# Kernel tuning notes

Hardware: AMD Instinct MI355X
Metric: run time of the kernel (lower is better)

The kernel has to match this reference:

```python
import jax, jax.numpy as jnp
import numpy as np

B = 16
C = 80
LEVELS = [(128, 128, 8), (64, 64, 16), (32, 32, 32), (16, 16, 64), (8, 8, 128)]
TOPN = 1000
MIN_SCORE = 0.05
NMS_THR = 0.6
MAX_OBJ = 100


def setup_inputs() -> dict:
    key = jax.random.key(0)
    inp = {}
    for l, (H, W, s) in enumerate(LEVELS):
        key, k1, k2, k3 = jax.random.split(key, 4)
        inp[f"cls{l}"] = jax.random.uniform(k1, (B, H, W, C), jnp.float32)
        inp[f"reg{l}"] = jax.random.uniform(k2, (B, H, W, 4), jnp.float32) * 128.0
        inp[f"ctr{l}"] = jax.random.uniform(k3, (B, H, W, 1), jnp.float32)
        xs = (jnp.arange(W, dtype=jnp.float32) + 0.5) * s
        ys = (jnp.arange(H, dtype=jnp.float32) + 0.5) * s
        gx, gy = jnp.meshgrid(xs, ys)  # [H, W]
        pos = jnp.stack([gx, gy], axis=-1)  # [H, W, 2]
        inp[f"pos{l}"] = jnp.broadcast_to(pos, (B, H, W, 2))
    return inp


def _nms_one(scores, classes, bboxes):
    # scores [N], classes int32 [N], bboxes float [N, 4] (already int-truncated values)
    s = jnp.where(scores > MIN_SCORE, scores, -jnp.inf)  # score-threshold mask
    top_s, top_i = jax.lax.top_k(s, TOPN)  # sort descending, keep topn
    top_c = jax.lax.stop_gradient(classes[top_i].astype(jnp.float32))
    top_b = bboxes[top_i]
    valid = top_s > MIN_SCORE
    wh = top_b[:, 2:4] - top_b[:, 0:2]
    areas = jnp.clip(wh[:, 0] * wh[:, 1], 0.0001)
    ar = jnp.arange(TOPN)

    def body(i, suppressed):
        active = valid[i] & (~suppressed[i])
        b = top_b[i]
        tl = jnp.maximum(b[0:2], top_b[:, 0:2])
        br = jnp.minimum(b[2:4], top_b[:, 2:4])
        owh = jnp.clip(br - tl, 0.0)
        inter = owh[:, 0] * owh[:, 1]
        union = jnp.clip(areas[i] + areas - inter, 0.0001)
        iou = inter / union
        return suppressed | (active & (ar > i) & (iou >= NMS_THR))

    suppressed = jax.lax.fori_loop(0, TOPN, body, jnp.zeros((TOPN,), bool))
    keep = valid & (~suppressed)
    rank = jnp.cumsum(keep.astype(jnp.int32)) - 1
    # scatter kept detections (in score order) into first MAX_OBJ slots; slot MAX_OBJ is a dump
    idx = jnp.where(keep & (rank < MAX_OBJ), rank, MAX_OBJ)
    out_s = jnp.full((MAX_OBJ + 1,), -1.0, jnp.float32).at[idx].set(jnp.where(keep, top_s, -1.0))[:MAX_OBJ]
    out_c = jnp.full((MAX_OBJ + 1,), -1.0, jnp.float32).at[idx].set(jnp.where(keep, top_c, -1.0))[:MAX_OBJ]
    out_b = jnp.zeros((MAX_OBJ + 1, 4), jnp.float32).at[idx].set(jnp.where(keep[:, None], top_b, 0.0))[:MAX_OBJ]
    return out_s, out_c, out_b


def _forward(cls_list, reg_list, ctr_list, pos_list):
    ss, cc, bb = [], [], []
    for c, r, t, p in zip(cls_list, reg_list, ctr_list, pos_list):
        b = c.shape[0]
        c = c.reshape(b, -1, c.shape[-1])   # [B, HW, 80]
        r = r.reshape(b, -1, 4)             # [B, HW, 4]
        t = t.reshape(b, -1)                # [B, HW]
        p = p.reshape(b, -1, 2)             # [B, HW, 2]
        sc = jnp.sqrt(jnp.max(c, axis=2) * t)
        cl = jnp.argmax(c, axis=2).astype(jnp.int32)
        bmin = p - r[:, :, 0:2]
        bmax = p + r[:, :, 2:4]
        # torch .int() truncates toward zero; values are used as floats afterward
        box = jax.lax.stop_gradient(jnp.trunc(jnp.concatenate([bmin, bmax], axis=2)))
        ss.append(sc); cc.append(cl); bb.append(box)
    scores = jnp.concatenate(ss, axis=1)
    classes = jnp.concatenate(cc, axis=1)
    boxes = jnp.concatenate(bb, axis=1)
    return jax.vmap(_nms_one)(scores, classes, boxes)


def reference(cls0, cls1, cls2, cls3, cls4, reg0, reg1, reg2, reg3, reg4,
              ctr0, ctr1, ctr2, ctr3, ctr4, pos0, pos1, pos2, pos3, pos4):
    return _forward([cls0, cls1, cls2, cls3, cls4],
                    [reg0, reg1, reg2, reg3, reg4],
                    [ctr0, ctr1, ctr2, ctr3, ctr4],
                    [pos0, pos1, pos2, pos3, pos4])
```

## Files before the change

kernel.cpp:

```cpp
#include <hip/hip_runtime.h>
#include <stdint.h>

typedef unsigned int u32;
typedef unsigned long long u64;

#define NTOT 21824
#define NBATCH 16
#define TOPN 1000
#define MAXOBJ 100
#define CAP 2048
#define CAPC 8192

__global__ void zero_kernel(u32* __restrict__ h) {
    int i = blockIdx.x * 1024 + threadIdx.x;
    if (i < NBATCH * 2048 + NBATCH * 32) h[i] = 0;
}

__global__ __launch_bounds__(256) void decode_kernel(
    const float* __restrict__ cls0, const float* __restrict__ cls1,
    const float* __restrict__ cls2, const float* __restrict__ cls3,
    const float* __restrict__ cls4,
    const float* __restrict__ ctr0, const float* __restrict__ ctr1,
    const float* __restrict__ ctr2, const float* __restrict__ ctr3,
    const float* __restrict__ ctr4,
    u32* __restrict__ keys, int* __restrict__ clsidx,
    u32* __restrict__ hist0)
{
    __shared__ u32 bh[2048];
    for (int i = threadIdx.x; i < 2048; i += 256) bh[i] = 0;
    __syncthreads();

    int tid = threadIdx.x;
    int g = tid >> 2, j = tid & 3;
    int loc = blockIdx.x * 64 + g;
    int b = blockIdx.y;
    if (loc < NTOT) {
        const float *cp, *tp;
        if (loc < 16384)      { size_t o = (size_t)b*16384 + loc;          cp = cls0 + o*80; tp = ctr0 + o; }
        else if (loc < 20480) { size_t o = (size_t)b*4096  + (loc-16384);  cp = cls1 + o*80; tp = ctr1 + o; }
        else if (loc < 21504) { size_t o = (size_t)b*1024  + (loc-20480);  cp = cls2 + o*80; tp = ctr2 + o; }
        else if (loc < 21760) { size_t o = (size_t)b*256   + (loc-21504);  cp = cls3 + o*80; tp = ctr3 + o; }
        else                  { size_t o = (size_t)b*64    + (loc-21760);  cp = cls4 + o*80; tp = ctr4 + o; }

        const float4* c4 = (const float4*)cp;
        float maxv = -1.0f; int arg = 0;
#pragma unroll
        for (int q = 0; q < 5; ++q) {
            float4 v = c4[j + 4*q];
            int ch = 16*q + 4*j;
            if (v.x > maxv) { maxv = v.x; arg = ch;     }
            if (v.y > maxv) { maxv = v.y; arg = ch + 1; }
            if (v.z > maxv) { maxv = v.z; arg = ch + 2; }
            if (v.w > maxv) { maxv = v.w; arg = ch + 3; }
        }
#pragma unroll
        for (int d = 1; d <= 2; d <<= 1) {
            float ov = __shfl_xor(maxv, d);
            int   oa = __shfl_xor(arg, d);
            if (ov > maxv || (ov == maxv && oa < arg)) { maxv = ov; arg = oa; }
        }
        if (j == 0) {
            float score = sqrtf(maxv * (*tp));
            u32 key = (score > 0.05f) ? (__float_as_uint(score) | 0x80000000u) : 0u;
            size_t o = (size_t)b * NTOT + loc;
            keys[o] = key;
            clsidx[o] = arg;
            if (key) atomicAdd(&bh[key >> 21], 1u);
        }
    }
    __syncthreads();
    for (int i = threadIdx.x; i < 2048; i += 256) {
        u32 c = bh[i];
        if (c) atomicAdd(&hist0[b * 2048 + i], c);
    }
}

__global__ __launch_bounds__(1024) void pivot_kernel(
    const u32* __restrict__ keys, const u32* __restrict__ hist0,
    u32* __restrict__ params,
    float* __restrict__ tscore, float* __restrict__ tcls, float4* __restrict__ tbox)
{
    __shared__ u32 shist[2048];
    __shared__ u32 s_wtot[16];
    __shared__ int s_tf;
    __shared__ u32 s_C, s_above;
    int b = blockIdx.x, tid = threadIdx.x;
    int lane = tid & 63, wave = tid >> 6;
    const u32* kb = keys + (size_t)b * NTOT;

    for (int i = tid; i < TOPN; i += 1024) {
        size_t o = (size_t)b * TOPN + i;
        tscore[o] = -1.0f; tcls[o] = -1.0f;
        tbox[o] = make_float4(0.f, 0.f, 0.f, 0.f);
    }

    u32 h0 = hist0[b * 2048 + 2 * tid];
    u32 h1 = hist0[b * 2048 + 2 * tid + 1];
    if (tid == 0) s_tf = -1;
    u32 x = h0 + h1;
#pragma unroll
    for (int off = 1; off < 64; off <<= 1) {
        u32 y = __shfl_down(x, off);
        if (lane + off < 64) x += y;
    }
    if (lane == 0) s_wtot[wave] = x;
    __syncthreads();
    u32 wsuf = 0, tot = 0;
    for (int w2 = 0; w2 < 16; ++w2) { u32 v = s_wtot[w2]; tot += v; if (w2 > wave) wsuf += v; }
    u32 suf0 = x + wsuf, suf1 = suf0 - h0;
    u32 target = (tot < TOPN) ? tot : TOPN;

    if (target > 0) {
        if (suf0 >= target) atomicMax(&s_tf, 2 * tid);
        if (suf1 >= target) atomicMax(&s_tf, 2 * tid + 1);
    }
    __syncthreads();
    int t0 = s_tf;
    if (target > 0) {
        if (2 * tid == t0)     { s_C = suf0; s_above = suf0 - h0; }
        if (2 * tid + 1 == t0) { s_C = suf1; s_above = suf1 - h1; }
    }
    __syncthreads();
    u32 C0 = (target > 0) ? s_C : 0;
    u32 above0 = (target > 0) ? s_above : 0;

    bool need2 = (target > 0 && C0 > CAP);
    int t1 = 0; u32 C1 = 0, above1 = 0;
    shist[2 * tid] = 0; shist[2 * tid + 1] = 0;
    if (tid == 0) s_tf = -1;
    __syncthreads();
    if (need2) {
        for (int i = tid; i < NTOT; i += 1024) {
            u32 k = kb[i];
            if (k && (int)(k >> 21) == t0) atomicAdd(&shist[(k >> 10) & 2047], 1u);
        }
    }
    __syncthreads();
    {
        u32 g0 = shist[2 * tid], g1 = shist[2 * tid + 1];
        u32 x2 = g0 + g1;
#pragma unroll
        for (int off = 1; off < 64; off <<= 1) {
            u32 y = __shfl_down(x2, off);
            if (lane + off < 64) x2 += y;
        }
        if (lane == 0) s_wtot[wave] = x2;
        __syncthreads();
        u32 ws2 = 0;
        for (int w2 = wave + 1; w2 < 16; ++w2) ws2 += s_wtot[w2];
        u32 sa0 = x2 + ws2, sa1 = sa0 - g0;
        u32 need2c = target - above0;
        if (need2) {
            if (sa0 >= need2c) atomicMax(&s_tf, 2 * tid);
            if (sa1 >= need2c) atomicMax(&s_tf, 2 * tid + 1);
        }
        __syncthreads();
        t1 = s_tf;
        if (need2) {
            if (2 * tid == t1)     { s_C = above0 + sa0; s_above = above0 + sa0 - g0; }
            if (2 * tid + 1 == t1) { s_C = above0 + sa1; s_above = above0 + sa1 - g1; }
        }
        __syncthreads();
        if (need2) { C1 = s_C; above1 = s_above; }
    }

    bool need3 = (need2 && C1 > CAP);
    int t2 = 0;
    __syncthreads();
    shist[2 * tid] = 0; shist[2 * tid + 1] = 0;
    if (tid == 0) s_tf = -1;
    __syncthreads();
    if (need3) {
        for (int i = tid; i < NTOT; i += 1024) {
            u32 k = kb[i];
            if (k && (int)(k >> 21) == t0 && (int)((k >> 10) & 2047) == t1)
                atomicAdd(&shist[k & 1023], 1u);
        }
    }
    __syncthreads();
    {
        u32 g = shist[tid];
        u32 x3 = g;
#pragma unroll
        for (int off = 1; off < 64; off <<= 1) {
            u32 y = __shfl_down(x3, off);
            if (lane + off < 64) x3 += y;
        }
        if (lane == 0) s_wtot[wave] = x3;
        __syncthreads();
        u32 ws3 = 0;
        for (int w2 = wave + 1; w2 < 16; ++w2) ws3 += s_wtot[w2];
        u32 sb = x3 + ws3;
        if (need3) {
            u32 need3c = target - above1;
            if (sb >= need3c && tid < 1024) atomicMax(&s_tf, tid);
        }
        __syncthreads();
        t2 = s_tf;
    }

    if (tid == 0) {
        u32 P;
        if (target == 0)      P = 0xFFFFFFFFu;
        else if (!need2)      P = (u32)t0 << 21;
        else if (!need3)      P = ((u32)t0 << 21) | ((u32)t1 << 10);
        else                  P = ((u32)t0 << 21) | ((u32)t1 << 10) | (u32)t2;
        params[2 * b] = P;
        params[2 * b + 1] = target;
    }
}

__global__ __launch_bounds__(256) void gather_kernel(
    const u32* __restrict__ keys, const u32* __restrict__ params,
    u64* __restrict__ candbuf, u32* __restrict__ gcnt)
{
    __shared__ u32 s_wcnt[4];
    __shared__ u32 s_base;
    int b = blockIdx.y;
    int tid = threadIdx.x;
    int lane = tid & 63, wave = tid >> 6;
    u32 P = params[2 * b];
    int i = blockIdx.x * 256 + tid;
    u32 k = (i < NTOT) ? keys[(size_t)b * NTOT + i] : 0u;
    bool pass = (k != 0u) && (k >= P);
    u64 mask = __ballot(pass);
    if (lane == 0) s_wcnt[wave] = (u32)__popcll(mask);
    __syncthreads();
    if (tid == 0) {
        u32 tot = s_wcnt[0] + s_wcnt[1] + s_wcnt[2] + s_wcnt[3];
        s_base = tot ? atomicAdd(&gcnt[b * 32], tot) : 0u;
    }
    __syncthreads();
    if (pass) {
        u32 woff = 0;
        for (int w2 = 0; w2 < wave; ++w2) woff += s_wcnt[w2];
        u32 pos = s_base + woff + (u32)__popcll(mask & ((1ull << lane) - 1ull));
        if (pos < CAPC)
            candbuf[(size_t)b * CAPC + pos] = ((u64)k << 32) | (u32)(~i);
    }
}

__global__ __launch_bounds__(256) void rank_kernel(
    const u64* __restrict__ candbuf, const u32* __restrict__ gcnt,
    const u32* __restrict__ params,
    const int* __restrict__ clsidx,
    const float* __restrict__ reg0, const float* __restrict__ reg1,
    const float* __restrict__ reg2, const float* __restrict__ reg3,
    const float* __restrict__ reg4,
    float* __restrict__ tscore, float* __restrict__ tcls, float4* __restrict__ tbox)
{
    int b = blockIdx.y;
    int lane = threadIdx.x & 63;
    u32 M = gcnt[b * 32]; if (M > CAPC) M = CAPC;
    u32 target = params[2 * b + 1];
    const u64* cb = candbuf + (size_t)b * CAPC;
    u32 Mr = (M + 63u) & ~63u;

    u32 wbase0 = blockIdx.x * 256 + (threadIdx.x & ~63u);
    for (u32 base = wbase0; base < M; base += 8 * 256) {
        u32 i0 = base + lane;
        bool val = (i0 < M);
        u64 e = val ? cb[i0] : ~0ull;
        u32 r = 0;
        for (u32 c0 = 0; c0 < Mr; c0 += 64) {
            u32 j = c0 + lane;
            u64 v = (j < M) ? cb[j] : 0ull;
            u32 vlo = (u32)v, vhi = (u32)(v >> 32);
#pragma unroll
            for (int s = 0; s < 64; ++s) {
                u32 lo = (u32)__builtin_amdgcn_readlane((int)vlo, s);
                u32 hi = (u32)__builtin_amdgcn_readlane((int)vhi, s);
                u64 vj = ((u64)hi << 32) | lo;
                r += (vj > e) ? 1u : 0u;
            }
        }
        if (val && r < target) {
            u32 k = (u32)(e >> 32);
            u32 loc = ~(u32)e;
            const float* rp; float st; u32 li; int wsh;
            if (loc < 16384u)      { li = loc;          wsh = 7; st = 8.f;   rp = reg0 + ((size_t)b*16384 + li)*4; }
            else if (loc < 20480u) { li = loc - 16384u; wsh = 6; st = 16.f;  rp = reg1 + ((size_t)b*4096  + li)*4; }
            else if (loc < 21504u) { li = loc - 20480u; wsh = 5; st = 32.f;  rp = reg2 + ((size_t)b*1024  + li)*4; }
            else if (loc < 21760u) { li = loc - 21504u; wsh = 4; st = 64.f;  rp = reg3 + ((size_t)b*256   + li)*4; }
            else                   { li = loc - 21760u; wsh = 3; st = 128.f; rp = reg4 + ((size_t)b*64    + li)*4; }
            u32 wx = li & ((1u << wsh) - 1u);
            u32 hy = li >> wsh;
            float px = ((float)wx + 0.5f) * st;
            float py = ((float)hy + 0.5f) * st;
            float4 rg = *(const float4*)rp;
            float4 bx;
            bx.x = truncf(px - rg.x); bx.y = truncf(py - rg.y);
            bx.z = truncf(px + rg.z); bx.w = truncf(py + rg.w);
            size_t src = (size_t)b * NTOT + loc;
            size_t o = (size_t)b * TOPN + r;
            tscore[o] = __uint_as_float(k & 0x7FFFFFFFu);
            tcls[o] = (float)clsidx[src];
            tbox[o] = bx;
        }
    }
}

__global__ __launch_bounds__(256) void iou_kernel(
    const float4* __restrict__ tbox, u64* __restrict__ sup)
{
    __shared__ float4 sbox[TOPN];
    int b = blockIdx.y;
    int tid = threadIdx.x, lane = tid & 63, wave = tid >> 6;
    const float4* tb = tbox + (size_t)b * TOPN;
    for (int i = tid; i < TOPN; i += 256) sbox[i] = tb[i];
    __syncthreads();
    int i = blockIdx.x * 4 + wave;
    float4 bi = sbox[i];
    float areai = fmaxf((bi.z - bi.x) * (bi.w - bi.y), 0.0001f);
    u64* row = sup + ((size_t)b * TOPN + i) * 16;
#pragma unroll
    for (int w = 0; w < 16; ++w) {
        int col = w * 64 + lane;
        bool bit = false;
        if (col < TOPN) {
            float4 bj = sbox[col];
            float areaj = fmaxf((bj.z - bj.x) * (bj.w - bj.y), 0.0001f);
            float tlx = fmaxf(bi.x, bj.x), tly = fmaxf(bi.y, bj.y);
            float brx = fminf(bi.z, bj.z), bry = fminf(bi.w, bj.w);
            float ow = fmaxf(brx - tlx, 0.f), oh = fmaxf(bry - tly, 0.f);
            float inter = ow * oh;
            float uni = fmaxf(areai + areaj - inter, 0.0001f);
            bit = (col > i) && (inter / uni >= 0.6f);
        }
        u64 m = __ballot(bit);
        if (lane == 0) row[w] = m;
    }
}

#define CHROWS 128
#define NCHUNK 8

__global__ __launch_bounds__(1024) void finalize_kernel(
    const float* __restrict__ tscore, const float* __restrict__ tcls,
    const float4* __restrict__ tbox, const u64* __restrict__ sup,
    float* __restrict__ out)
{
    __shared__ u64 mat[2][CHROWS * 16];
    __shared__ u32 validsh[TOPN];
    __shared__ u64 removed_sh[16];
    __shared__ u32 wpref[17];
    int b = blockIdx.x, tid = threadIdx.x;
    int wave = tid >> 6, lane = tid & 63;

    for (int i = tid; i < TOPN; i += 1024)
        validsh[i] = (tscore[(size_t)b * TOPN + i] > 0.05f) ? 1u : 0u;

    const u64* supb = sup + (size_t)b * TOPN * 16;
    for (int idx = tid; idx < CHROWS * 16; idx += 1024)
        mat[0][idx] = supb[idx];
    __syncthreads();

    u64 my = 0;
    if (wave == 0) {
#pragma unroll
        for (int w2 = 0; w2 < 16; ++w2) {
            int i = w2 * 64 + lane;
            bool v = (i < TOPN) ? (validsh[i] != 0) : false;
            u64 m = __ballot(v);
            if (lane == w2) my = ~m;
        }
    }

    for (int chunk = 0; chunk < NCHUNK; ++chunk) {
        if (wave > 0 && chunk + 1 < NCHUNK) {
            int nr = (chunk + 1 == NCHUNK - 1) ? (TOPN - (NCHUNK - 1) * CHROWS) : CHROWS;
            const u64* src = supb + (size_t)(chunk + 1) * CHROWS * 16;
            u64* dst = mat[(chunk + 1) & 1];
            for (int idx = tid - 64; idx < nr * 16; idx += 960)
                dst[idx] = src[idx];
        }
        if (wave == 0) {
            int r0 = chunk * CHROWS;
            int rows = (chunk == NCHUNK - 1) ? (TOPN - r0) : CHROWS;
            int lw = lane & 15;
            const u64* M = mat[chunk & 1];
            for (int sub = 0; sub < rows; sub += 64) {
                int w2 = (r0 + sub) >> 6;
                u64 cur = __shfl(my, w2);
                int nsub = rows - sub; if (nsub > 64) nsub = 64;
                const u64* R = M + sub * 16;
                int ngrp = nsub >> 3;
                u64 cme[8], cww[8];
#pragma unroll
                for (int g = 0; g < 8; ++g) { cme[g] = R[g*16 + lw]; cww[g] = R[g*16 + w2]; }
                for (int grp = 0; grp < ngrp; ++grp) {
                    u64 nme[8] = {0,0,0,0,0,0,0,0}, nww[8] = {0,0,0,0,0,0,0,0};
                    if (grp + 1 < ngrp) {
                        const u64* Rn = R + (grp + 1) * 128;
#pragma unroll
                        for (int g = 0; g < 8; ++g) { nme[g] = Rn[g*16 + lw]; nww[g] = Rn[g*16 + w2]; }
                    }
#pragma unroll
                    for (int g = 0; g < 8; ++g) {
                        int u = grp * 8 + g;
                        u64 bit = (cur >> u) & 1ull;
                        u64 act = bit - 1ull;
                        cur |= cww[g] & act;
                        my  |= cme[g] & act;
                    }
#pragma unroll
                    for (int g = 0; g < 8; ++g) { cme[g] = nme[g]; cww[g] = nww[g]; }
                }
            }
        }
        __syncthreads();
    }
    if (wave == 0) {
        if (lane < 16) removed_sh[lane] = my;
        u32 pc = (lane < 16) ? (u32)__popcll(~my) : 0u;
#pragma unroll
        for (int off = 1; off < 16; off <<= 1) {
            u32 y = __shfl_up(pc, off);
            if (lane >= off) pc += y;
        }
        if (lane < 16) wpref[lane + 1] = pc;
        if (lane == 0) wpref[0] = 0;
    }
    __syncthreads();

    float* out_s = out;
    float* out_c = out + NBATCH * MAXOBJ;
    float* out_b = out + 2 * NBATCH * MAXOBJ;
    if (tid < MAXOBJ)     { out_s[b * MAXOBJ + tid] = -1.f; out_c[b * MAXOBJ + tid] = -1.f; }
    if (tid < MAXOBJ * 4) out_b[b * MAXOBJ * 4 + tid] = 0.f;
    __syncthreads();
    if (tid < TOPN) {
        u64 kw = ~removed_sh[tid >> 6];
        if ((kw >> (tid & 63)) & 1ull) {
            int rank = (int)wpref[tid >> 6] + (int)__popcll(kw & ((1ull << (tid & 63)) - 1ull));
            if (rank < MAXOBJ) {
                size_t o = (size_t)b * TOPN + tid;
                out_s[b * MAXOBJ + rank] = tscore[o];
                out_c[b * MAXOBJ + rank] = tcls[o];
                ((float4*)out_b)[b * MAXOBJ + rank] = tbox[o];
            }
        }
    }
}

extern "C" void kernel_launch(void* const* d_in, const int* in_sizes, int n_in,
                              void* d_out, int out_size, void* d_ws, size_t ws_size,
                              hipStream_t stream) {
    (void)in_sizes; (void)n_in; (void)out_size; (void)ws_size;
    const float* cls[5]; const float* reg[5]; const float* ctr[5];
    for (int l = 0; l < 5; ++l) {
        cls[l] = (const float*)d_in[4 * l + 0];
        reg[l] = (const float*)d_in[4 * l + 1];
        ctr[l] = (const float*)d_in[4 * l + 2];
    }
    char* w = (char*)d_ws;
    u32*    keys   = (u32*)(w + 0);
    int*    clsidx = (int*)(w + 1396736);
    float*  tscore = (float*)(w + 8380416);
    float*  tcls   = (float*)(w + 8444416);
    float4* tbox   = (float4*)(w + 8508416);
    u64*    sup    = (u64*)(w + 8764416);
    u64*    candbuf= (u64*)(w + 8764416);
    u32*    hist0  = (u32*)(w + 9812992);
    u32*    gcnt   = (u32*)(w + 9944064);
    u32*    params = (u32*)(w + 9946112);

    zero_kernel<<<33, 1024, 0, stream>>>(hist0);
    decode_kernel<<<dim3((NTOT + 63) / 64, NBATCH), 256, 0, stream>>>(
        cls[0], cls[1], cls[2], cls[3], cls[4],
        ctr[0], ctr[1], ctr[2], ctr[3], ctr[4],
        keys, clsidx, hist0);
    pivot_kernel<<<NBATCH, 1024, 0, stream>>>(keys, hist0, params, tscore, tcls, tbox);
    gather_kernel<<<dim3((NTOT + 255) / 256, NBATCH), 256, 0, stream>>>(keys, params, candbuf, gcnt);
    rank_kernel<<<dim3(8, NBATCH), 256, 0, stream>>>(candbuf, gcnt, params, clsidx,
                                                     reg[0], reg[1], reg[2], reg[3], reg[4],
                                                     tscore, tcls, tbox);
    iou_kernel<<<dim3(TOPN / 4, NBATCH), 256, 0, stream>>>(tbox, sup);
    finalize_kernel<<<NBATCH, 1024, 0, stream>>>(tscore, tcls, tbox, sup, (float*)d_out);
}
```

Baseline: 278.0 us.

## Fuse histogram, zeroing and gather into pivot kernel with candidate compaction

Removes the zero kernel and the global histogram atomics from decode. The pivot kernel now builds the first-level histogram itself, using four per-wave-group shared histograms to reduce atomic contention. It then compacts top-bucket candidates into a buffer that later radix passes rescan instead of the full key array, and does the final gather itself. This drops two kernel launches and the global atomics, but puts more serial work onto only 16 blocks.

```diff
diff --git a/kernel.cpp b/kernel.cpp
--- a/kernel.cpp
+++ b/kernel.cpp
@@ -10,11 +10,6 @@
 #define MAXOBJ 100
 #define CAP 2048
 #define CAPC 8192
-
-__global__ void zero_kernel(u32* __restrict__ h) {
-    int i = blockIdx.x * 1024 + threadIdx.x;
-    if (i < NBATCH * 2048 + NBATCH * 32) h[i] = 0;
-}
 
 __global__ __launch_bounds__(256) void decode_kernel(
     const float* __restrict__ cls0, const float* __restrict__ cls1,
@@ -23,70 +18,61 @@
     const float* __restrict__ ctr0, const float* __restrict__ ctr1,
     const float* __restrict__ ctr2, const float* __restrict__ ctr3,
     const float* __restrict__ ctr4,
-    u32* __restrict__ keys, int* __restrict__ clsidx,
-    u32* __restrict__ hist0)
+    u32* __restrict__ keys, int* __restrict__ clsidx)
 {
-    __shared__ u32 bh[2048];
-    for (int i = threadIdx.x; i < 2048; i += 256) bh[i] = 0;
-    __syncthreads();
-
     int tid = threadIdx.x;
     int g = tid >> 2, j = tid & 3;
     int loc = blockIdx.x * 64 + g;
     int b = blockIdx.y;
-    if (loc < NTOT) {
-        const float *cp, *tp;
-        if (loc < 16384)      { size_t o = (size_t)b*16384 + loc;          cp = cls0 + o*80; tp = ctr0 + o; }
-        else if (loc < 20480) { size_t o = (size_t)b*4096  + (loc-16384);  cp = cls1 + o*80; tp = ctr1 + o; }
-        else if (loc < 21504) { size_t o = (size_t)b*1024  + (loc-20480);  cp = cls2 + o*80; tp = ctr2 + o; }
-        else if (loc < 21760) { size_t o = (size_t)b*256   + (loc-21504);  cp = cls3 + o*80; tp = ctr3 + o; }
-        else                  { size_t o = (size_t)b*64    + (loc-21760);  cp = cls4 + o*80; tp = ctr4 + o; }
-
-        const float4* c4 = (const float4*)cp;
-        float maxv = -1.0f; int arg = 0;
-#pragma unroll
-        for (int q = 0; q < 5; ++q) {
-            float4 v = c4[j + 4*q];
-            int ch = 16*q + 4*j;
-            if (v.x > maxv) { maxv = v.x; arg = ch;     }
-            if (v.y > maxv) { maxv = v.y; arg = ch + 1; }
-            if (v.z > maxv) { maxv = v.z; arg = ch + 2; }
-            if (v.w > maxv) { maxv = v.w; arg = ch + 3; }
-        }
-#pragma unroll
-        for (int d = 1; d <= 2; d <<= 1) {
-            float ov = __shfl_xor(maxv, d);
-            int   oa = __shfl_xor(arg, d);
-            if (ov > maxv || (ov == maxv && oa < arg)) { maxv = ov; arg = oa; }
-        }
-        if (j == 0) {
-            float score = sqrtf(maxv * (*tp));
-            u32 key = (score > 0.05f) ? (__float_as_uint(score) | 0x80000000u) : 0u;
-            size_t o = (size_t)b * NTOT + loc;
-            keys[o] = key;
-            clsidx[o] = arg;
-            if (key) atomicAdd(&bh[key >> 21], 1u);
-        }
-    }
-    __syncthreads();
-    for (int i = threadIdx.x; i < 2048; i += 256) {
-        u32 c = bh[i];
-        if (c) atomicAdd(&hist0[b * 2048 + i], c);
+    if (loc >= NTOT) return;
+    const float *cp, *tp;
+    if (loc < 16384)      { size_t o = (size_t)b*16384 + loc;          cp = cls0 + o*80; tp = ctr0 + o; }
+    else if (loc < 20480) { size_t o = (size_t)b*4096  + (loc-16384);  cp = cls1 + o*80; tp = ctr1 + o; }
+    else if (loc < 21504) { size_t o = (size_t)b*1024  + (loc-20480);  cp = cls2 + o*80; tp = ctr2 + o; }
+    else if (loc < 21760) { size_t o = (size_t)b*256   + (loc-21504);  cp = cls3 + o*80; tp = ctr3 + o; }
+    else                  { size_t o = (size_t)b*64    + (loc-21760);  cp = cls4 + o*80; tp = ctr4 + o; }
+
+    const float4* c4 = (const float4*)cp;
+    float maxv = -1.0f; int arg = 0;
+#pragma unroll
+    for (int q = 0; q < 5; ++q) {
+        float4 v = c4[j + 4*q];
+        int ch = 16*q + 4*j;
+        if (v.x > maxv) { maxv = v.x; arg = ch;     }
+        if (v.y > maxv) { maxv = v.y; arg = ch + 1; }
+        if (v.z > maxv) { maxv = v.z; arg = ch + 2; }
+        if (v.w > maxv) { maxv = v.w; arg = ch + 3; }
+    }
+#pragma unroll
+    for (int d = 1; d <= 2; d <<= 1) {
+        float ov = __shfl_xor(maxv, d);
+        int   oa = __shfl_xor(arg, d);
+        if (ov > maxv || (ov == maxv && oa < arg)) { maxv = ov; arg = oa; }
+    }
+    if (j == 0) {
+        float score = sqrtf(maxv * (*tp));
+        u32 key = (score > 0.05f) ? (__float_as_uint(score) | 0x80000000u) : 0u;
+        size_t o = (size_t)b * NTOT + loc;
+        keys[o] = key;
+        clsidx[o] = arg;
     }
 }
 
 __global__ __launch_bounds__(1024) void pivot_kernel(
-    const u32* __restrict__ keys, const u32* __restrict__ hist0,
-    u32* __restrict__ params,
+    const u32* __restrict__ keys,
+    u64* __restrict__ cb, u64* __restrict__ cand2,
+    u32* __restrict__ gcnt, u32* __restrict__ params,
     float* __restrict__ tscore, float* __restrict__ tcls, float4* __restrict__ tbox)
 {
-    __shared__ u32 shist[2048];
+    __shared__ u32 h4[4][2048];
     __shared__ u32 s_wtot[16];
     __shared__ int s_tf;
-    __shared__ u32 s_C, s_above;
+    __shared__ u32 s_C, s_above, s_cnt;
     int b = blockIdx.x, tid = threadIdx.x;
-    int lane = tid & 63, wave = tid >> 6;
+    int lane = tid & 63, wave = tid >> 6, sub = wave & 3;
     const u32* kb = keys + (size_t)b * NTOT;
+    u64* cbb = cb + (size_t)b * CAPC;
+    u64* c2b = cand2 + (size_t)b * CAPC;
 
     for (int i = tid; i < TOPN; i += 1024) {
         size_t o = (size_t)b * TOPN + i;
@@ -94,9 +80,16 @@
         tbox[o] = make_float4(0.f, 0.f, 0.f, 0.f);
     }
 
-    u32 h0 = hist0[b * 2048 + 2 * tid];
-    u32 h1 = hist0[b * 2048 + 2 * tid + 1];
-    if (tid == 0) s_tf = -1;
+    for (int i = tid; i < 4 * 2048; i += 1024) ((u32*)h4)[i] = 0;
+    if (tid == 0) { s_tf = -1; s_cnt = 0; }
+    __syncthreads();
+    for (int i = tid; i < NTOT; i += 1024) {
+        u32 k = kb[i];
+        if (k) atomicAdd(&h4[sub][k >> 21], 1u);
+    }
+    __syncthreads();
+    u32 h0 = h4[0][2*tid] + h4[1][2*tid] + h4[2][2*tid] + h4[3][2*tid];
+    u32 h1 = h4[0][2*tid+1] + h4[1][2*tid+1] + h4[2][2*tid+1] + h4[3][2*tid+1];
     u32 x = h0 + h1;
 #pragma unroll
     for (int off = 1; off < 64; off <<= 1) {
@@ -109,7 +102,6 @@
     for (int w2 = 0; w2 < 16; ++w2) { u32 v = s_wtot[w2]; tot += v; if (w2 > wave) wsuf += v; }
     u32 suf0 = x + wsuf, suf1 = suf0 - h0;
     u32 target = (tot < TOPN) ? tot : TOPN;
-
     if (target > 0) {
         if (suf0 >= target) atomicMax(&s_tf, 2 * tid);
         if (suf1 >= target) atomicMax(&s_tf, 2 * tid + 1);
@@ -123,21 +115,49 @@
     __syncthreads();
     u32 C0 = (target > 0) ? s_C : 0;
     u32 above0 = (target > 0) ? s_above : 0;
+    bool useCand = (C0 <= CAPC);
+
+    for (int base = 0; base < NTOT; base += 1024) {
+        int i = base + tid;
+        u32 k = (i < NTOT) ? kb[i] : 0u;
+        bool pass = (target > 0) && k && ((int)(k >> 21) >= t0);
+        u64 mask = __ballot(pass);
+        u32 wcnt = (u32)__popcll(mask);
+        u32 wbase = 0;
+        if (lane == 0 && wcnt) wbase = atomicAdd(&s_cnt, wcnt);
+        wbase = __shfl(wbase, 0);
+        if (pass) {
+            u32 pos = wbase + (u32)__popcll(mask & ((1ull << lane) - 1ull));
+            if (pos < CAPC) cbb[pos] = ((u64)k << 32) | (u32)(~i);
+        }
+    }
+    __syncthreads();
+    u32 C0g = s_cnt; (void)C0g;
+    __syncthreads();
+    if (tid == 0) s_cnt = 0;
 
     bool need2 = (target > 0 && C0 > CAP);
     int t1 = 0; u32 C1 = 0, above1 = 0;
-    shist[2 * tid] = 0; shist[2 * tid + 1] = 0;
+    for (int i = tid; i < 4 * 2048; i += 1024) ((u32*)h4)[i] = 0;
     if (tid == 0) s_tf = -1;
     __syncthreads();
     if (need2) {
-        for (int i = tid; i < NTOT; i += 1024) {
-            u32 k = kb[i];
-            if (k && (int)(k >> 21) == t0) atomicAdd(&shist[(k >> 10) & 2047], 1u);
+        if (useCand) {
+            for (u32 i = tid; i < C0; i += 1024) {
+                u32 k = (u32)(cbb[i] >> 32);
+                if ((int)(k >> 21) == t0) atomicAdd(&h4[sub][(k >> 10) & 2047], 1u);
+            }
+        } else {
+            for (int i = tid; i < NTOT; i += 1024) {
+                u32 k = kb[i];
+                if (k && (int)(k >> 21) == t0) atomicAdd(&h4[sub][(k >> 10) & 2047], 1u);
+            }
         }
     }
     __syncthreads();
     {
-        u32 g0 = shist[2 * tid], g1 = shist[2 * tid + 1];
+        u32 g0 = h4[0][2*tid] + h4[1][2*tid] + h4[2][2*tid] + h4[3][2*tid];
+        u32 g1 = h4[0][2*tid+1] + h4[1][2*tid+1] + h4[2][2*tid+1] + h4[3][2*tid+1];
         u32 x2 = g0 + g1;
 #pragma unroll
         for (int off = 1; off < 64; off <<= 1) {
@@ -167,20 +187,29 @@
     bool need3 = (need2 && C1 > CAP);
     int t2 = 0;
     __syncthreads();
-    shist[2 * tid] = 0; shist[2 * tid + 1] = 0;
+    for (int i = tid; i < 4 * 2048; i += 1024) ((u32*)h4)[i] = 0;
     if (tid == 0) s_tf = -1;
     __syncthreads();
     if (need3) {
-        for (int i = tid; i < NTOT; i += 1024) {
-            u32 k = kb[i];
-            if (k && (int)(k >> 21) == t0 && (int)((k >> 10) & 2047) == t1)
-                atomicAdd(&shist[k & 1023], 1u);
+        if (useCand) {
+            for (u32 i = tid; i < C0; i += 1024) {
+                u32 k = (u32)(cbb[i] >> 32);
+                if ((int)(k >> 21) == t0 && (int)((k >> 10) & 2047) == t1)
+                    atomicAdd(&h4[sub][k & 1023], 1u);
+            }
+        } else {
+            for (int i = tid; i < NTOT; i += 1024) {
+                u32 k = kb[i];
+                if (k && (int)(k >> 21) == t0 && (int)((k >> 10) & 2047) == t1)
+                    atomicAdd(&h4[sub][k & 1023], 1u);
+            }
         }
     }
     __syncthreads();
     {
-        u32 g = shist[tid];
-        u32 x3 = g;
+        u32 g0 = h4[0][2*tid] + h4[1][2*tid] + h4[2][2*tid] + h4[3][2*tid];
+        u32 g1 = h4[0][2*tid+1] + h4[1][2*tid+1] + h4[2][2*tid+1] + h4[3][2*tid+1];
+        u32 x3 = g0 + g1;
 #pragma unroll
         for (int off = 1; off < 64; off <<= 1) {
             u32 y = __shfl_down(x3, off);
@@ -190,58 +219,65 @@
         __syncthreads();
         u32 ws3 = 0;
         for (int w2 = wave + 1; w2 < 16; ++w2) ws3 += s_wtot[w2];
-        u32 sb = x3 + ws3;
+        u32 sb0 = x3 + ws3, sb1 = sb0 - g0;
         if (need3) {
             u32 need3c = target - above1;
-            if (sb >= need3c && tid < 1024) atomicMax(&s_tf, tid);
+            if (sb0 >= need3c) atomicMax(&s_tf, 2 * tid);
+            if (sb1 >= need3c) atomicMax(&s_tf, 2 * tid + 1);
         }
         __syncthreads();
         t2 = s_tf;
     }
 
+    u32 P;
+    if (target == 0) P = 0xFFFFFFFFu;
+    else if (!need2) P = (u32)t0 << 21;
+    else if (!need3) P = ((u32)t0 << 21) | ((u32)t1 << 10);
+    else             P = ((u32)t0 << 21) | ((u32)t1 << 10) | (u32)t2;
+
+    if (useCand) {
+        u32 Cr = (C0 + 1023u) & ~1023u;
+        for (u32 base = 0; base < Cr; base += 1024) {
+            u32 i = base + tid;
+            u64 e = 0; bool pass = false;
+            if (i < C0 && target > 0) { e = cbb[i]; pass = ((u32)(e >> 32) >= P); }
+            u64 mask = __ballot(pass);
+            u32 wcnt = (u32)__popcll(mask);
+            u32 wbase = 0;
+            if (lane == 0 && wcnt) wbase = atomicAdd(&s_cnt, wcnt);
+            wbase = __shfl(wbase, 0);
+            if (pass) {
+                u32 pos = wbase + (u32)__popcll(mask & ((1ull << lane) - 1ull));
+                if (pos < CAPC) c2b[pos] = e;
+            }
+        }
+    } else {
+        for (int base = 0; base < NTOT; base += 1024) {
+            int i = base + tid;
+            u32 k = (i < NTOT) ? kb[i] : 0u;
+            bool pass = (target > 0) && k && (k >= P);
+            u64 mask = __ballot(pass);
+            u32 wcnt = (u32)__popcll(mask);
+            u32 wbase = 0;
+            if (lane == 0 && wcnt) wbase = atomicAdd(&s_cnt, wcnt);
+            wbase = __shfl(wbase, 0);
+            if (pass) {
+                u32 pos = wbase + (u32)__popcll(mask & ((1ull << lane) - 1ull));
+                if (pos < CAPC) c2b[pos] = ((u64)k << 32) | (u32)(~i);
+            }
+        }
+    }
+    __syncthreads();
     if (tid == 0) {
-        u32 P;
-        if (target == 0)      P = 0xFFFFFFFFu;
-        else if (!need2)      P = (u32)t0 << 21;
-        else if (!need3)      P = ((u32)t0 << 21) | ((u32)t1 << 10);
-        else                  P = ((u32)t0 << 21) | ((u32)t1 << 10) | (u32)t2;
+        u32 M = s_cnt; if (M > CAPC) M = CAPC;
+        gcnt[b * 32] = M;
         params[2 * b] = P;
         params[2 * b + 1] = target;
     }
 }
 
-__global__ __launch_bounds__(256) void gather_kernel(
-    const u32* __restrict__ keys, const u32* __restrict__ params,
-    u64* __restrict__ candbuf, u32* __restrict__ gcnt)
-{
-    __shared__ u32 s_wcnt[4];
-    __shared__ u32 s_base;
-    int b = blockIdx.y;
-    int tid = threadIdx.x;
-    int lane = tid & 63, wave = tid >> 6;
-    u32 P = params[2 * b];
-    int i = blockIdx.x * 256 + tid;
-    u32 k = (i < NTOT) ? keys[(size_t)b * NTOT + i] : 0u;
-    bool pass = (k != 0u) && (k >= P);
-    u64 mask = __ballot(pass);
-    if (lane == 0) s_wcnt[wave] = (u32)__popcll(mask);
-    __syncthreads();
-    if (tid == 0) {
-        u32 tot = s_wcnt[0] + s_wcnt[1] + s_wcnt[2] + s_wcnt[3];
-        s_base = tot ? atomicAdd(&gcnt[b * 32], tot) : 0u;
-    }
-    __syncthreads();
-    if (pass) {
-        u32 woff = 0;
-        for (int w2 = 0; w2 < wave; ++w2) woff += s_wcnt[w2];
-        u32 pos = s_base + woff + (u32)__popcll(mask & ((1ull << lane) - 1ull));
-        if (pos < CAPC)
-            candbuf[(size_t)b * CAPC + pos] = ((u64)k << 32) | (u32)(~i);
-    }
-}
-
 __global__ __launch_bounds__(256) void rank_kernel(
-    const u64* __restrict__ candbuf, const u32* __restrict__ gcnt,
+    const u64* __restrict__ cand2, const u32* __restrict__ gcnt,
     const u32* __restrict__ params,
     const int* __restrict__ clsidx,
     const float* __restrict__ reg0, const float* __restrict__ reg1,
@@ -253,7 +289,7 @@
     int lane = threadIdx.x & 63;
     u32 M = gcnt[b * 32]; if (M > CAPC) M = CAPC;
     u32 target = params[2 * b + 1];
-    const u64* cb = candbuf + (size_t)b * CAPC;
+    const u64* cb = cand2 + (size_t)b * CAPC;
     u32 Mr = (M + 63u) & ~63u;
 
     u32 wbase0 = blockIdx.x * 256 + (threadIdx.x & ~63u);
@@ -456,23 +492,22 @@
     char* w = (char*)d_ws;
     u32*    keys   = (u32*)(w + 0);
     int*    clsidx = (int*)(w + 1396736);
+    u64*    cb     = (u64*)(w + 2793472);
+    u64*    cand2  = (u64*)(w + 3842048);
     float*  tscore = (float*)(w + 8380416);
     float*  tcls   = (float*)(w + 8444416);
     float4* tbox   = (float4*)(w + 8508416);
     u64*    sup    = (u64*)(w + 8764416);
-    u64*    candbuf= (u64*)(w + 8764416);
-    u32*    hist0  = (u32*)(w + 9812992);
     u32*    gcnt   = (u32*)(w + 9944064);
     u32*    params = (u32*)(w + 9946112);
 
-    zero_kernel<<<33, 1024, 0, stream>>>(hist0);
     decode_kernel<<<dim3((NTOT + 63) / 64, NBATCH), 256, 0, stream>>>(
         cls[0], cls[1], cls[2], cls[3], cls[4],
         ctr[0], ctr[1], ctr[2], ctr[3], ctr[4],
-        keys, clsidx, hist0);
-    pivot_kernel<<<NBATCH, 1024, 0, stream>>>(keys, hist0, params, tscore, tcls, tbox);
-    gather_kernel<<<dim3((NTOT + 255) / 256, NBATCH), 256, 0, stream>>>(keys, params, candbuf, gcnt);
-    rank_kernel<<<dim3(8, NBATCH), 256, 0, stream>>>(candbuf, gcnt, params, clsidx,
+        keys, clsidx);
+    pivot_kernel<<<NBATCH, 1024, 0, stream>>>(keys, cb, cand2, gcnt, params,
+                                              tscore, tcls, tbox);
+    rank_kernel<<<dim3(8, NBATCH), 256, 0, stream>>>(cand2, gcnt, params, clsidx,
                                                      reg[0], reg[1], reg[2], reg[3], reg[4],
                                                      tscore, tcls, tbox);
     iou_kernel<<<dim3(TOPN / 4, NBATCH), 256, 0, stream>>>(tbox, sup);
```

Result: no change. 283.4 us (+1.9%).
